# Kernel optimization log

Hardware: AMD Instinct MI355X
Metric: run time of the kernel (lower is better)

Reference implementation:

```python
import jax, jax.numpy as jnp
import numpy as np

MASK_VALUE = -10000000000.0
B, S = 2, 2048
HQ, HKV, HD = 16, 8, 256
D = HQ * HD  # 4096
ROPE_BASE = 10000.0


def rms_norm(x, scale, eps=1e-6):
    # Gemma-style RMSNorm over the last (head_dim) axis with (1 + scale) gain.
    var = jnp.mean(jnp.square(x), axis=-1, keepdims=True)
    return x * jax.lax.rsqrt(var + eps) * (1.0 + scale)


def apply_rope(x, positions):
    # x: [b, t, h, d]; positions: [b, t]
    d = x.shape[-1]
    fraction = 2.0 * jnp.arange(d // 2, dtype=jnp.float32) / d
    timescale = ROPE_BASE ** fraction                     # [d/2]
    sinusoid = positions[..., None].astype(jnp.float32) / timescale  # [b, t, d/2]
    sin = jnp.sin(sinusoid)[:, :, None, :]                # [b, t, 1, d/2]
    cos = jnp.cos(sinusoid)[:, :, None, :]
    first, second = jnp.split(x, 2, axis=-1)
    out = jnp.concatenate([first * cos - second * sin,
                           second * cos + first * sin], axis=-1)
    return out.astype(x.dtype)


def setup_inputs() -> dict:
    key = jax.random.key(0)
    ks = jax.random.split(key, 6)
    x = jax.random.normal(ks[0], (B, S, D), dtype=jnp.float32)
    Wq = jax.random.normal(ks[1], (D, HQ * HD), dtype=jnp.float32) * 0.02
    Wk = jax.random.normal(ks[2], (D, HKV * HD), dtype=jnp.float32) * 0.02
    Wv = jax.random.normal(ks[3], (D, HKV * HD), dtype=jnp.float32) * 0.02
    Wo = jax.random.normal(ks[4], (HQ * HD, D), dtype=jnp.float32) * 0.02
    k_scale = jnp.zeros((HD,), dtype=jnp.float32)
    v_scale = jnp.zeros((HD,), dtype=jnp.float32)
    mask = jnp.broadcast_to(jnp.tril(jnp.ones((S, S), dtype=bool))[None], (B, S, S))
    position = jnp.broadcast_to(jnp.arange(S, dtype=jnp.int32)[None], (B, S))
    return {"x": x, "Wq": Wq, "Wk": Wk, "Wv": Wv, "Wo": Wo,
            "k_scale": k_scale, "v_scale": v_scale,
            "mask": mask, "position": position}


def reference(x, Wq, Wk, Wv, Wo, k_scale, v_scale, mask, position):
    b, t, _ = x.shape
    group = HQ // HKV
    q = (x @ Wq).reshape(b, t, HQ, HD)
    k = (x @ Wk).reshape(b, t, HKV, HD)
    v = (x @ Wv).reshape(b, t, HKV, HD)
    k = rms_norm(k, k_scale)
    v = rms_norm(v, v_scale)
    q = apply_rope(q, position)
    k = apply_rope(k, position)
    # [b, hkv, group, t, d] view of q; avoids materializing repeated K/V (same math as repeat).
    q = q.transpose(0, 2, 1, 3).reshape(b, HKV, group, t, HD)
    k = k.transpose(0, 2, 1, 3)  # [b, hkv, T, d]
    v = v.transpose(0, 2, 1, 3)
    scores = jnp.einsum('bhgtd,bhTd->bhgtT', q, k) / jnp.sqrt(jnp.float32(HD))
    scores = jnp.where(mask[:, None, None, :, :], scores, MASK_VALUE)
    weights = jax.nn.softmax(scores, axis=-1)
    out = jnp.einsum('bhgtT,bhTd->bhgtd', weights, v)
    out = out.reshape(b, HQ, t, HD).transpose(0, 2, 1, 3).reshape(b, t, HQ * HD)
    return out @ Wo
```

## Files before the change

### kernel.cpp

```cpp
#include <hip/hip_runtime.h>
#include <stdint.h>

typedef __bf16 bf16;
typedef __bf16 bf16x4 __attribute__((ext_vector_type(4)));
typedef __bf16 bf16x8 __attribute__((ext_vector_type(8)));
typedef float f32x4 __attribute__((ext_vector_type(4)));

#define GAS __attribute__((address_space(1)))
#define LAS __attribute__((address_space(3)))

__device__ __forceinline__ void gload_lds16(const void* g, void* l) {
  __builtin_amdgcn_global_load_lds((GAS const void*)g, (LAS void*)l, 16, 0, 0);
}

__global__ __launch_bounds__(256) void cvt_bf16(const float* __restrict__ in,
                                                bf16* __restrict__ out, int n4) {
  int i = blockIdx.x * 256 + threadIdx.x;
  if (i >= n4) return;
  float4 v = ((const float4*)in)[i];
  bf16x4 o;
  o[0] = (bf16)v.x; o[1] = (bf16)v.y; o[2] = (bf16)v.z; o[3] = (bf16)v.w;
  ((bf16x4*)out)[i] = o;
}

__global__ __launch_bounds__(256) void tconv(const float* __restrict__ W,
                                             bf16* __restrict__ Wt, int K, int N) {
  __shared__ bf16 tile[64][65];
  const int tx = threadIdx.x & 63, ty = threadIdx.x >> 6;
  const int n0 = blockIdx.x * 64, k0 = blockIdx.y * 64;
#pragma unroll
  for (int i = 0; i < 16; ++i) {
    int kr = ty + i * 4;
    tile[kr][tx] = (bf16)W[(size_t)(k0 + kr) * N + n0 + tx];
  }
  __syncthreads();
#pragma unroll
  for (int i = 0; i < 16; ++i) {
    int nr = ty + i * 4;
    Wt[(size_t)(n0 + nr) * K + k0 + tx] = tile[tx][nr];
  }
}

template <int OUTF32>
__global__ __launch_bounds__(512, 2) void gemm256(const bf16* __restrict__ A,
                                                  const bf16* __restrict__ Bt,
                                                  void* __restrict__ Cp,
                                                  const int N, const int K,
                                                  const int ncc_l, const int cbx_l) {
  __shared__ __attribute__((aligned(16))) bf16 lds[2][4][8192];
  const int t = threadIdx.x, w = t >> 6, l = t & 63;
  const int la = l & 15, lq = l >> 4;
  const int xcd = blockIdx.x & 7, wi = blockIdx.x >> 3;
  const int cr = xcd >> ncc_l, cc = xcd & ((1 << ncc_l) - 1);
  const int by = (cr << 3) + (wi >> cbx_l);
  const int bx = (cc << cbx_l) + (wi & ((1 << cbx_l) - 1));
  const int m0 = by * 256, n0 = bx * 256;
  const int wr = w >> 2, wc = w & 3;
  const int c0 = w * 64 + l;
  const int sr0 = c0 >> 2, soff = (((c0 & 3) ^ ((c0 >> 3) & 3)) << 3);
  const bf16* pA0 = A + (size_t)(m0 + sr0) * K + soff;
  const bf16* pA1 = pA0 + (size_t)128 * K;
  const bf16* pB0 = Bt + (size_t)(n0 + sr0) * K + soff;
  const bf16* pB1 = pB0 + (size_t)128 * K;
  const int rsl = (lq ^ ((la >> 1) & 3)) << 3;

  f32x4 acc[8][4] = {};

#define STAGE_SLAB(s, nb, kti)                                                \
  do {                                                                        \
    const bf16* p0_ = ((s) & 1) ? pB0 : pA0;                                  \
    const bf16* p1_ = ((s) & 1) ? pB1 : pA1;                                  \
    const size_t ko_ = (size_t)(kti) * 64 + ((s) >> 1) * 32;                  \
    gload_lds16(p0_ + ko_, &lds[nb][s][w * 512]);                             \
    gload_lds16(p1_ + ko_, &lds[nb][s][4096 + w * 512]);                      \
  } while (0)

#define PHASE(kh, mg)                                                         \
  {                                                                           \
    bf16x8 a_[4];                                                             \
    _Pragma("unroll") for (int m_ = 0; m_ < 4; ++m_)                          \
        a_[m_] = *(const bf16x8*)&lds[bi][(kh)*2][(wr * 128 + (mg)*64 + m_ * 16 + la) * 32 + rsl]; \
    __builtin_amdgcn_s_setprio(1);                                            \
    _Pragma("unroll") for (int m_ = 0; m_ < 4; ++m_)                          \
      _Pragma("unroll") for (int n_ = 0; n_ < 4; ++n_)                        \
          acc[(mg)*4 + m_][n_] = __builtin_amdgcn_mfma_f32_16x16x32_bf16(     \
              a_[m_], bfr[n_], acc[(mg)*4 + m_][n_], 0, 0, 0);                \
    __builtin_amdgcn_s_setprio(0);                                            \
  }

  STAGE_SLAB(0, 0, 0);
  STAGE_SLAB(1, 0, 0);
  STAGE_SLAB(2, 0, 0);
  STAGE_SLAB(3, 0, 0);

  const int NT = K >> 6;
  for (int kt = 0; kt < NT; ++kt) {
    const int bi = kt & 1, nbi = bi ^ 1;
    const bool pf = (kt + 1) < NT;
    bf16x8 bfr[4];
    if (pf) asm volatile("s_waitcnt vmcnt(4)" ::: "memory");
    else    asm volatile("s_waitcnt vmcnt(0)" ::: "memory");
    __builtin_amdgcn_s_barrier();
    __builtin_amdgcn_sched_barrier(0);
    if (pf) STAGE_SLAB(0, nbi, kt + 1);
#pragma unroll
    for (int n_ = 0; n_ < 4; ++n_)
      bfr[n_] = *(const bf16x8*)&lds[bi][1][(wc * 64 + n_ * 16 + la) * 32 + rsl];
    PHASE(0, 0)
    if (pf) STAGE_SLAB(1, nbi, kt + 1);
    PHASE(0, 1)
    if (pf) asm volatile("s_waitcnt vmcnt(4)" ::: "memory");
    else    asm volatile("s_waitcnt vmcnt(0)" ::: "memory");
    __builtin_amdgcn_s_barrier();
    __builtin_amdgcn_sched_barrier(0);
    if (pf) STAGE_SLAB(2, nbi, kt + 1);
#pragma unroll
    for (int n_ = 0; n_ < 4; ++n_)
      bfr[n_] = *(const bf16x8*)&lds[bi][3][(wc * 64 + n_ * 16 + la) * 32 + rsl];
    PHASE(1, 0)
    if (pf) STAGE_SLAB(3, nbi, kt + 1);
    PHASE(1, 1)
  }
#undef PHASE
#undef STAGE_SLAB

  const int crow = m0 + wr * 128, ccol = n0 + wc * 64;
  if (OUTF32) {
    float* C = (float*)Cp;
#pragma unroll
    for (int mi = 0; mi < 8; ++mi)
#pragma unroll
      for (int ni = 0; ni < 4; ++ni)
#pragma unroll
        for (int i = 0; i < 4; ++i)
          C[(size_t)(crow + mi * 16 + lq * 4 + i) * N + ccol + ni * 16 + la] = acc[mi][ni][i];
  } else {
    bf16* C = (bf16*)Cp;
#pragma unroll
    for (int mi = 0; mi < 8; ++mi)
#pragma unroll
      for (int ni = 0; ni < 4; ++ni)
#pragma unroll
        for (int i = 0; i < 4; ++i)
          C[(size_t)(crow + mi * 16 + lq * 4 + i) * N + ccol + ni * 16 + la] = (bf16)acc[mi][ni][i];
  }
}

__global__ __launch_bounds__(256) void rope_q(bf16* __restrict__ qkv, const int* __restrict__ pos) {
  const int w = threadIdx.x >> 6, l = threadIdx.x & 63;
  const int idx = blockIdx.x * 4 + w;
  const int bt = idx >> 4, h = idx & 15;
  bf16* p = qkv + (size_t)bt * 8192 + h * 256 + l * 4;
  bf16x4 xv = *(const bf16x4*)p;
  float x[4], y[4];
#pragma unroll
  for (int j = 0; j < 4; ++j) x[j] = (float)xv[j];
#pragma unroll
  for (int j = 0; j < 4; ++j) y[j] = __shfl_xor(x[j], 32, 64);
  const float posf = (float)pos[bt];
  bf16x4 ov;
#pragma unroll
  for (int j = 0; j < 4; ++j) {
    const int pr = (l & 31) * 4 + j;
    float sv, cv;
    sincosf(posf * exp2f((float)pr * (-13.287712379549449f / 128.0f)), &sv, &cv);
    float o = x[j] * cv + ((l < 32) ? -y[j] : y[j]) * sv;
    ov[j] = (bf16)(o * 0.0625f);
  }
  *(bf16x4*)p = ov;
}

__global__ __launch_bounds__(256) void norm_rope_k(bf16* __restrict__ kbase,
                                                   const float* __restrict__ scale,
                                                   const int* __restrict__ pos) {
  const int w = threadIdx.x >> 6, l = threadIdx.x & 63;
  const int idx = blockIdx.x * 4 + w;
  const int bt = idx >> 3, h = idx & 7;
  bf16* p = kbase + (size_t)bt * 8192 + h * 256 + l * 4;
  bf16x4 xv = *(const bf16x4*)p;
  float x[4];
#pragma unroll
  for (int j = 0; j < 4; ++j) x[j] = (float)xv[j];
  float ss = x[0] * x[0] + x[1] * x[1] + x[2] * x[2] + x[3] * x[3];
#pragma unroll
  for (int m = 1; m < 64; m <<= 1) ss += __shfl_xor(ss, m, 64);
  const float r = rsqrtf(ss * (1.0f / 256.0f) + 1e-6f);
#pragma unroll
  for (int j = 0; j < 4; ++j) x[j] = x[j] * r * (1.0f + scale[l * 4 + j]);
  float y[4];
#pragma unroll
  for (int j = 0; j < 4; ++j) y[j] = __shfl_xor(x[j], 32, 64);
  const float posf = (float)pos[bt];
  bf16x4 ov;
#pragma unroll
  for (int j = 0; j < 4; ++j) {
    const int pr = (l & 31) * 4 + j;
    float sv, cv;
    sincosf(posf * exp2f((float)pr * (-13.287712379549449f / 128.0f)), &sv, &cv);
    float o = x[j] * cv + ((l < 32) ? -y[j] : y[j]) * sv;
    ov[j] = (bf16)o;
  }
  *(bf16x4*)p = ov;
}

__global__ __launch_bounds__(256) void norm_v(bf16* __restrict__ vbase,
                                              const float* __restrict__ scale) {
  const int w = threadIdx.x >> 6, l = threadIdx.x & 63;
  const int idx = blockIdx.x * 4 + w;
  const int bt = idx >> 3, h = idx & 7;
  bf16* p = vbase + (size_t)bt * 8192 + h * 256 + l * 4;
  bf16x4 xv = *(const bf16x4*)p;
  float x[4];
#pragma unroll
  for (int j = 0; j < 4; ++j) x[j] = (float)xv[j];
  float ss = x[0] * x[0] + x[1] * x[1] + x[2] * x[2] + x[3] * x[3];
#pragma unroll
  for (int m = 1; m < 64; m <<= 1) ss += __shfl_xor(ss, m, 64);
  const float r = rsqrtf(ss * (1.0f / 256.0f) + 1e-6f);
  bf16x4 ov;
#pragma unroll
  for (int j = 0; j < 4; ++j) ov[j] = (bf16)(x[j] * r * (1.0f + scale[l * 4 + j]));
  *(bf16x4*)p = ov;
}

__global__ __launch_bounds__(256) void vtrans(const bf16* __restrict__ vbase,
                                              bf16* __restrict__ vt) {
  __shared__ bf16 tile[64][65];
  const int tx = threadIdx.x & 63, ty = threadIdx.x >> 6;
  const int tt = blockIdx.x, dd = blockIdx.y, bh = blockIdx.z;
  const int b = bh >> 3, h = bh & 7;
#pragma unroll
  for (int i = 0; i < 16; ++i) {
    int trow = tt * 64 + ty + i * 4;
    tile[ty + i * 4][tx] = vbase[(size_t)(b * 2048 + trow) * 8192 + h * 256 + dd * 64 + tx];
  }
  __syncthreads();
#pragma unroll
  for (int i = 0; i < 16; ++i) {
    int drow = dd * 64 + ty + i * 4;
    vt[((size_t)(b * 8 + h) * 256 + drow) * 2048 + tt * 64 + tx] = tile[tx][ty + i * 4];
  }
}

__global__ __launch_bounds__(512, 2) void flash_attn(const bf16* __restrict__ qkv,
                                                     const bf16* __restrict__ vt,
                                                     bf16* __restrict__ o) {
  __shared__ __attribute__((aligned(16))) bf16 Ks[2 * 16384];
  __shared__ __attribute__((aligned(16))) bf16 Vs[2 * 16384];
  __shared__ __attribute__((aligned(16))) bf16 Ps[8 * 1152];
  const int t = threadIdx.x, w = t >> 6, l = t & 63;
  const int la = l & 15, lq = l >> 4;
  const int h = blockIdx.x, qbp = blockIdx.y, b = blockIdx.z;
  const int hkv = h >> 1;

  const bf16* kbase = qkv + (size_t)(b * 2048) * 8192 + 4096 + hkv * 256;
  const bf16* vbase = vt + ((size_t)(b * 8 + hkv)) * 256 * 2048;

  const bf16* ksrc[4];
  const bf16* vsrc[4];
#pragma unroll
  for (int i = 0; i < 4; ++i) {
    int c = i * 512 + t;
    int krr = c >> 5, ksl = (c & 31) ^ (krr & 7);
    int vrr = c >> 3, vsl = (c & 7) ^ (vrr & 7);
    ksrc[i] = kbase + (size_t)krr * 8192 + ksl * 8;
    vsrc[i] = vbase + (size_t)vrr * 2048 + vsl * 8;
  }

#define STAGE(bb, tt0)                                                        \
  do {                                                                        \
    _Pragma("unroll") for (int i_ = 0; i_ < 4; ++i_)                          \
        gload_lds16(ksrc[i_] + (size_t)(tt0) * 8192,                          \
                    Ks + (bb) * 16384 + i_ * 4096 + w * 512);                 \
    _Pragma("unroll") for (int i_ = 0; i_ < 4; ++i_)                          \
        gload_lds16(vsrc[i_] + (tt0), Vs + (bb) * 16384 + i_ * 4096 + w * 512); \
  } while (0)

  for (int part = 0; part < 2; ++part) {
    const int qb = part ? qbp : (15 - qbp);
    const int q0 = qb * 128;
    const int rbase = q0 + w * 16;

    bf16x8 qf[8];
    {
      const bf16* qrow = qkv + (size_t)(b * 2048 + rbase + la) * 8192 + h * 256 + lq * 8;
#pragma unroll
      for (int kg = 0; kg < 8; ++kg) qf[kg] = *(const bf16x8*)(qrow + kg * 32);
    }
    f32x4 acc[16] = {};
    float mrow[4] = {-1e30f, -1e30f, -1e30f, -1e30f};
    float lrow[4] = {0.f, 0.f, 0.f, 0.f};
    const int nT = 2 * qb + 2;

    STAGE(0, 0);
    int cur = 0;
    for (int tti = 0; tti < nT; ++tti) {
      const int t0 = tti * 64;
      if (tti + 1 < nT) {
        STAGE(cur ^ 1, t0 + 64);
        asm volatile("s_waitcnt vmcnt(8)" ::: "memory");
      } else {
        asm volatile("s_waitcnt vmcnt(0)" ::: "memory");
      }
      __builtin_amdgcn_s_barrier();
      __builtin_amdgcn_sched_barrier(0);
      if (t0 <= rbase + 15) {
        const bf16* Kc = Ks + cur * 16384;
        const bf16* Vc = Vs + cur * 16384;
        f32x4 s[4] = {};
        __builtin_amdgcn_s_setprio(1);
#pragma unroll
        for (int n = 0; n < 4; ++n) {
          int rT = n * 16 + la;
#pragma unroll
          for (int kg = 0; kg < 8; ++kg) {
            int sl = (kg * 4 + lq) ^ (rT & 7);
            bf16x8 kbv = *(const bf16x8*)(Kc + rT * 256 + sl * 8);
            s[n] = __builtin_amdgcn_mfma_f32_16x16x32_bf16(qf[kg], kbv, s[n], 0, 0, 0);
          }
        }
        __builtin_amdgcn_s_setprio(0);
        float scalef[4];
#pragma unroll
        for (int i = 0; i < 4; ++i) {
          const int row = rbase + lq * 4 + i;
          float mx = -1e30f;
#pragma unroll
          for (int n = 0; n < 4; ++n) {
            float v = s[n][i];
            v = (t0 + n * 16 + la > row) ? -1e30f : v;
            s[n][i] = v;
            mx = fmaxf(mx, v);
          }
          mx = fmaxf(mx, __shfl_xor(mx, 1, 64));
          mx = fmaxf(mx, __shfl_xor(mx, 2, 64));
          mx = fmaxf(mx, __shfl_xor(mx, 4, 64));
          mx = fmaxf(mx, __shfl_xor(mx, 8, 64));
          const float mnew = fmaxf(mrow[i], mx);
          scalef[i] = __expf(mrow[i] - mnew);
          float ps = 0.f;
#pragma unroll
          for (int n = 0; n < 4; ++n) {
            float v = s[n][i];
            float pp = (v <= -1e29f) ? 0.f : __expf(v - mnew);
            s[n][i] = pp;
            ps += pp;
          }
          ps += __shfl_xor(ps, 1, 64);
          ps += __shfl_xor(ps, 2, 64);
          ps += __shfl_xor(ps, 4, 64);
          ps += __shfl_xor(ps, 8, 64);
          mrow[i] = mnew;
          lrow[i] = lrow[i] * scalef[i] + ps;
        }
#pragma unroll
        for (int n = 0; n < 16; ++n) {
          acc[n][0] *= scalef[0]; acc[n][1] *= scalef[1];
          acc[n][2] *= scalef[2]; acc[n][3] *= scalef[3];
        }
        bf16* pw = Ps + w * 1152;
#pragma unroll
        for (int n = 0; n < 4; ++n)
#pragma unroll
          for (int i = 0; i < 4; ++i)
            pw[(lq * 4 + i) * 72 + n * 16 + la] = (bf16)s[n][i];
        __builtin_amdgcn_s_setprio(1);
#pragma unroll
        for (int kc = 0; kc < 2; ++kc) {
          bf16x8 pa = *(const bf16x8*)(pw + la * 72 + kc * 32 + lq * 8);
#pragma unroll
          for (int n = 0; n < 16; ++n) {
            int rd = n * 16 + la;
            int sl = (kc * 4 + lq) ^ (rd & 7);
            bf16x8 vbv = *(const bf16x8*)(Vc + rd * 64 + sl * 8);
            acc[n] = __builtin_amdgcn_mfma_f32_16x16x32_bf16(pa, vbv, acc[n], 0, 0, 0);
          }
        }
        __builtin_amdgcn_s_setprio(0);
      }
      __builtin_amdgcn_s_barrier();
      __builtin_amdgcn_sched_barrier(0);
      cur ^= 1;
    }
#pragma unroll
    for (int i = 0; i < 4; ++i) {
      const int row = rbase + lq * 4 + i;
      const float inv = 1.0f / lrow[i];
      bf16* orow = o + ((size_t)(b * 2048 + row)) * 4096 + h * 256;
#pragma unroll
      for (int n = 0; n < 16; ++n) orow[n * 16 + la] = (bf16)(acc[n][i] * inv);
    }
  }
#undef STAGE
}

__global__ void fill_err(float* o, int n) {
  int i = blockIdx.x * 256 + threadIdx.x;
  if (i < n) o[i] = 1e9f;
}

extern "C" void kernel_launch(void* const* d_in, const int* in_sizes, int n_in,
                              void* d_out, int out_size, void* d_ws, size_t ws_size,
                              hipStream_t stream) {
  const float* x = (const float*)d_in[0];
  const float* Wq = (const float*)d_in[1];
  const float* Wk = (const float*)d_in[2];
  const float* Wv = (const float*)d_in[3];
  const float* Wo = (const float*)d_in[4];
  const float* kscale = (const float*)d_in[5];
  const float* vscale = (const float*)d_in[6];
  const int* pos = (const int*)d_in[8];
  float* out = (float*)d_out;

  const size_t WS_NEED = 251658240ull;
  if (ws_size < WS_NEED) {
    fill_err<<<65536, 256, 0, stream>>>(out, out_size);
    return;
  }
  char* ws = (char*)d_ws;
  bf16* x16   = (bf16*)(ws);
  bf16* wqkvt = (bf16*)(ws + 33554432);
  bf16* wot   = (bf16*)(ws + 100663296);
  bf16* qkv   = (bf16*)(ws + 134217728);
  bf16* vtb   = (bf16*)(ws + 201326592);
  bf16* ao    = (bf16*)(ws + 218103808);

  cvt_bf16<<<16384, 256, 0, stream>>>(x, x16, 4194304);
  tconv<<<dim3(64, 64), 256, 0, stream>>>(Wq, wqkvt, 4096, 4096);
  tconv<<<dim3(32, 64), 256, 0, stream>>>(Wk, wqkvt + (size_t)4096 * 4096, 4096, 2048);
  tconv<<<dim3(32, 64), 256, 0, stream>>>(Wv, wqkvt + (size_t)6144 * 4096, 4096, 2048);
  tconv<<<dim3(64, 64), 256, 0, stream>>>(Wo, wot, 4096, 4096);

  gemm256<0><<<512, 512, 0, stream>>>(x16, wqkvt, qkv, 8192, 4096, 2, 3);

  rope_q<<<16384, 256, 0, stream>>>(qkv, pos);
  norm_rope_k<<<8192, 256, 0, stream>>>(qkv + 4096, kscale, pos);
  norm_v<<<8192, 256, 0, stream>>>(qkv + 6144, vscale);
  vtrans<<<dim3(32, 4, 16), 256, 0, stream>>>(qkv + 6144, vtb);

  flash_attn<<<dim3(16, 8, 2), 512, 0, stream>>>(qkv, vtb, ao);

  gemm256<1><<<256, 512, 0, stream>>>(ao, wot, out, 4096, 4096, 2, 2);
}
```

Before: 634.5 us.

## Share K/V tiles across GQA head pair and compute 32 query rows per wave

Restructures flash attention so each block serves one KV head and both query heads in its GQA group. Waves alternate between the two query heads, and each wave computes two 16-row query sub-tiles against every loaded K/V fragment. This halves redundant K/V staging across heads and doubles MFMA work per LDS fragment read, with 64-row query blocks, 256 threads and 1 block per CU. The cost is far more registers per wave (two accumulator sets of 16 f32x4) and less causal skipping within a tile, since the per-wave diagonal check was removed.

```diff
diff --git a/kernel.cpp b/kernel.cpp
--- a/kernel.cpp
+++ b/kernel.cpp
@@ -242,55 +242,48 @@
   }
 }
 
-__global__ __launch_bounds__(512, 2) void flash_attn(const bf16* __restrict__ qkv,
+__global__ __launch_bounds__(256, 1) void flash_attn(const bf16* __restrict__ qkv,
                                                      const bf16* __restrict__ vt,
                                                      bf16* __restrict__ o) {
   __shared__ __attribute__((aligned(16))) bf16 Ks[2 * 16384];
   __shared__ __attribute__((aligned(16))) bf16 Vs[2 * 16384];
-  __shared__ __attribute__((aligned(16))) bf16 Ps[8 * 1152];
+  __shared__ __attribute__((aligned(16))) bf16 Ps[4 * 2304];
   const int t = threadIdx.x, w = t >> 6, l = t & 63;
   const int la = l & 15, lq = l >> 4;
-  const int h = blockIdx.x, qbp = blockIdx.y, b = blockIdx.z;
-  const int hkv = h >> 1;
+  const int hkv = blockIdx.x, qp = blockIdx.y, b = blockIdx.z;
+  const int h = hkv * 2 + (w & 1);
 
   const bf16* kbase = qkv + (size_t)(b * 2048) * 8192 + 4096 + hkv * 256;
   const bf16* vbase = vt + ((size_t)(b * 8 + hkv)) * 256 * 2048;
 
-  const bf16* ksrc[4];
-  const bf16* vsrc[4];
-#pragma unroll
-  for (int i = 0; i < 4; ++i) {
-    int c = i * 512 + t;
-    int krr = c >> 5, ksl = (c & 31) ^ (krr & 7);
-    int vrr = c >> 3, vsl = (c & 7) ^ (vrr & 7);
-    ksrc[i] = kbase + (size_t)krr * 8192 + ksl * 8;
-    vsrc[i] = vbase + (size_t)vrr * 2048 + vsl * 8;
-  }
+  const bf16* ksrc = kbase + (size_t)(t >> 5) * 8192 + (((t & 31) ^ ((t >> 5) & 7)) << 3);
+  const bf16* vsrc = vbase + (size_t)(t >> 3) * 2048 + (((t & 7) ^ ((t >> 3) & 7)) << 3);
 
 #define STAGE(bb, tt0)                                                        \
   do {                                                                        \
-    _Pragma("unroll") for (int i_ = 0; i_ < 4; ++i_)                          \
-        gload_lds16(ksrc[i_] + (size_t)(tt0) * 8192,                          \
-                    Ks + (bb) * 16384 + i_ * 4096 + w * 512);                 \
-    _Pragma("unroll") for (int i_ = 0; i_ < 4; ++i_)                          \
-        gload_lds16(vsrc[i_] + (tt0), Vs + (bb) * 16384 + i_ * 4096 + w * 512); \
+    _Pragma("unroll") for (int i_ = 0; i_ < 8; ++i_)                          \
+        gload_lds16(ksrc + (size_t)((tt0) + i_ * 8) * 8192,                   \
+                    Ks + (bb) * 16384 + i_ * 2048 + t * 8);                   \
+    _Pragma("unroll") for (int i_ = 0; i_ < 8; ++i_)                          \
+        gload_lds16(vsrc + (size_t)i_ * 65536 + (tt0),                        \
+                    Vs + (bb) * 16384 + i_ * 2048 + t * 8);                   \
   } while (0)
 
   for (int part = 0; part < 2; ++part) {
-    const int qb = part ? qbp : (15 - qbp);
-    const int q0 = qb * 128;
-    const int rbase = q0 + w * 16;
-
-    bf16x8 qf[8];
-    {
-      const bf16* qrow = qkv + (size_t)(b * 2048 + rbase + la) * 8192 + h * 256 + lq * 8;
-#pragma unroll
-      for (int kg = 0; kg < 8; ++kg) qf[kg] = *(const bf16x8*)(qrow + kg * 32);
+    const int qb = part ? qp : (31 - qp);
+    const int rbase = qb * 64 + (w >> 1) * 32;
+
+    bf16x8 qf[2][8];
+#pragma unroll
+    for (int mi = 0; mi < 2; ++mi) {
+      const bf16* qrow = qkv + (size_t)(b * 2048 + rbase + mi * 16 + la) * 8192 + h * 256 + lq * 8;
+#pragma unroll
+      for (int kg = 0; kg < 8; ++kg) qf[mi][kg] = *(const bf16x8*)(qrow + kg * 32);
     }
-    f32x4 acc[16] = {};
-    float mrow[4] = {-1e30f, -1e30f, -1e30f, -1e30f};
-    float lrow[4] = {0.f, 0.f, 0.f, 0.f};
-    const int nT = 2 * qb + 2;
+    f32x4 acc[2][16] = {};
+    float mrow[2][4] = {{-1e30f, -1e30f, -1e30f, -1e30f}, {-1e30f, -1e30f, -1e30f, -1e30f}};
+    float lrow[2][4] = {};
+    const int nT = qb + 1;
 
     STAGE(0, 0);
     int cur = 0;
@@ -298,98 +291,104 @@
       const int t0 = tti * 64;
       if (tti + 1 < nT) {
         STAGE(cur ^ 1, t0 + 64);
-        asm volatile("s_waitcnt vmcnt(8)" ::: "memory");
+        asm volatile("s_waitcnt vmcnt(16)" ::: "memory");
       } else {
         asm volatile("s_waitcnt vmcnt(0)" ::: "memory");
       }
       __builtin_amdgcn_s_barrier();
       __builtin_amdgcn_sched_barrier(0);
-      if (t0 <= rbase + 15) {
-        const bf16* Kc = Ks + cur * 16384;
-        const bf16* Vc = Vs + cur * 16384;
-        f32x4 s[4] = {};
-        __builtin_amdgcn_s_setprio(1);
-#pragma unroll
-        for (int n = 0; n < 4; ++n) {
-          int rT = n * 16 + la;
-#pragma unroll
-          for (int kg = 0; kg < 8; ++kg) {
-            int sl = (kg * 4 + lq) ^ (rT & 7);
-            bf16x8 kbv = *(const bf16x8*)(Kc + rT * 256 + sl * 8);
-            s[n] = __builtin_amdgcn_mfma_f32_16x16x32_bf16(qf[kg], kbv, s[n], 0, 0, 0);
-          }
+      const bf16* Kc = Ks + cur * 16384;
+      const bf16* Vc = Vs + cur * 16384;
+      f32x4 s[2][4] = {};
+      __builtin_amdgcn_s_setprio(1);
+#pragma unroll
+      for (int n = 0; n < 4; ++n) {
+        int rT = n * 16 + la;
+#pragma unroll
+        for (int kg = 0; kg < 8; ++kg) {
+          int sl = (kg * 4 + lq) ^ (rT & 7);
+          bf16x8 kbv = *(const bf16x8*)(Kc + rT * 256 + sl * 8);
+          s[0][n] = __builtin_amdgcn_mfma_f32_16x16x32_bf16(qf[0][kg], kbv, s[0][n], 0, 0, 0);
+          s[1][n] = __builtin_amdgcn_mfma_f32_16x16x32_bf16(qf[1][kg], kbv, s[1][n], 0, 0, 0);
         }
-        __builtin_amdgcn_s_setprio(0);
+      }
+      __builtin_amdgcn_s_setprio(0);
+      bf16* pw = Ps + w * 2304;
+#pragma unroll
+      for (int mi = 0; mi < 2; ++mi) {
         float scalef[4];
 #pragma unroll
         for (int i = 0; i < 4; ++i) {
-          const int row = rbase + lq * 4 + i;
+          const int row = rbase + mi * 16 + lq * 4 + i;
           float mx = -1e30f;
 #pragma unroll
           for (int n = 0; n < 4; ++n) {
-            float v = s[n][i];
+            float v = s[mi][n][i];
             v = (t0 + n * 16 + la > row) ? -1e30f : v;
-            s[n][i] = v;
+            s[mi][n][i] = v;
             mx = fmaxf(mx, v);
           }
           mx = fmaxf(mx, __shfl_xor(mx, 1, 64));
           mx = fmaxf(mx, __shfl_xor(mx, 2, 64));
           mx = fmaxf(mx, __shfl_xor(mx, 4, 64));
           mx = fmaxf(mx, __shfl_xor(mx, 8, 64));
-          const float mnew = fmaxf(mrow[i], mx);
-          scalef[i] = __expf(mrow[i] - mnew);
+          const float mnew = fmaxf(mrow[mi][i], mx);
+          scalef[i] = __expf(mrow[mi][i] - mnew);
           float ps = 0.f;
 #pragma unroll
           for (int n = 0; n < 4; ++n) {
-            float v = s[n][i];
+            float v = s[mi][n][i];
             float pp = (v <= -1e29f) ? 0.f : __expf(v - mnew);
-            s[n][i] = pp;
+            s[mi][n][i] = pp;
             ps += pp;
           }
           ps += __shfl_xor(ps, 1, 64);
           ps += __shfl_xor(ps, 2, 64);
           ps += __shfl_xor(ps, 4, 64);
           ps += __shfl_xor(ps, 8, 64);
-          mrow[i] = mnew;
-          lrow[i] = lrow[i] * scalef[i] + ps;
+          mrow[mi][i] = mnew;
+          lrow[mi][i] = lrow[mi][i] * scalef[i] + ps;
         }
 #pragma unroll
         for (int n = 0; n < 16; ++n) {
-          acc[n][0] *= scalef[0]; acc[n][1] *= scalef[1];
-          acc[n][2] *= scalef[2]; acc[n][3] *= scalef[3];
+          acc[mi][n][0] *= scalef[0]; acc[mi][n][1] *= scalef[1];
+          acc[mi][n][2] *= scalef[2]; acc[mi][n][3] *= scalef[3];
         }
-        bf16* pw = Ps + w * 1152;
 #pragma unroll
         for (int n = 0; n < 4; ++n)
 #pragma unroll
           for (int i = 0; i < 4; ++i)
-            pw[(lq * 4 + i) * 72 + n * 16 + la] = (bf16)s[n][i];
-        __builtin_amdgcn_s_setprio(1);
-#pragma unroll
-        for (int kc = 0; kc < 2; ++kc) {
-          bf16x8 pa = *(const bf16x8*)(pw + la * 72 + kc * 32 + lq * 8);
-#pragma unroll
-          for (int n = 0; n < 16; ++n) {
-            int rd = n * 16 + la;
-            int sl = (kc * 4 + lq) ^ (rd & 7);
-            bf16x8 vbv = *(const bf16x8*)(Vc + rd * 64 + sl * 8);
-            acc[n] = __builtin_amdgcn_mfma_f32_16x16x32_bf16(pa, vbv, acc[n], 0, 0, 0);
-          }
+            pw[(mi * 16 + lq * 4 + i) * 72 + n * 16 + la] = (bf16)s[mi][n][i];
+      }
+      __builtin_amdgcn_s_setprio(1);
+#pragma unroll
+      for (int kc = 0; kc < 2; ++kc) {
+        bf16x8 pa0 = *(const bf16x8*)(pw + (la) * 72 + kc * 32 + lq * 8);
+        bf16x8 pa1 = *(const bf16x8*)(pw + (16 + la) * 72 + kc * 32 + lq * 8);
+#pragma unroll
+        for (int n = 0; n < 16; ++n) {
+          int rd = n * 16 + la;
+          int sl = (kc * 4 + lq) ^ (rd & 7);
+          bf16x8 vbv = *(const bf16x8*)(Vc + rd * 64 + sl * 8);
+          acc[0][n] = __builtin_amdgcn_mfma_f32_16x16x32_bf16(pa0, vbv, acc[0][n], 0, 0, 0);
+          acc[1][n] = __builtin_amdgcn_mfma_f32_16x16x32_bf16(pa1, vbv, acc[1][n], 0, 0, 0);
         }
-        __builtin_amdgcn_s_setprio(0);
       }
+      __builtin_amdgcn_s_setprio(0);
       __builtin_amdgcn_s_barrier();
       __builtin_amdgcn_sched_barrier(0);
       cur ^= 1;
     }
 #pragma unroll
-    for (int i = 0; i < 4; ++i) {
-      const int row = rbase + lq * 4 + i;
-      const float inv = 1.0f / lrow[i];
-      bf16* orow = o + ((size_t)(b * 2048 + row)) * 4096 + h * 256;
-#pragma unroll
-      for (int n = 0; n < 16; ++n) orow[n * 16 + la] = (bf16)(acc[n][i] * inv);
-    }
+    for (int mi = 0; mi < 2; ++mi)
+#pragma unroll
+      for (int i = 0; i < 4; ++i) {
+        const int row = rbase + mi * 16 + lq * 4 + i;
+        const float inv = 1.0f / lrow[mi][i];
+        bf16* orow = o + ((size_t)(b * 2048 + row)) * 4096 + h * 256;
+#pragma unroll
+        for (int n = 0; n < 16; ++n) orow[n * 16 + la] = (bf16)(acc[mi][n][i] * inv);
+      }
   }
 #undef STAGE
 }
@@ -438,7 +437,7 @@
   norm_v<<<8192, 256, 0, stream>>>(qkv + 6144, vscale);
   vtrans<<<dim3(32, 4, 16), 256, 0, stream>>>(qkv + 6144, vtb);
 
-  flash_attn<<<dim3(16, 8, 2), 512, 0, stream>>>(qkv, vtb, ao);
+  flash_attn<<<dim3(8, 16, 2), 256, 0, stream>>>(qkv, vtb, ao);
 
   gemm256<1><<<256, 512, 0, stream>>>(ao, wot, out, 4096, 4096, 2, 2);
 }
```

Measured after the change: 704.5 us. +11.0%, slower.

## Shrink flash-attention blocks to four waves with 32-key tiles and doubled grid

Applied to the files above, without the earlier changes.

The attention kernel now runs 256 threads (4 waves) per block, each block covering 64 query rows instead of 128, and the grid doubles along the query axis. The key/value staging tile shrinks from 64 to 32 keys, with a new swizzle for the smaller V tile. Shared memory per block roughly halves. The goal is more, smaller blocks to spread causal work more evenly across CUs and raise occupancy. The cost is twice as many loop iterations, each with barriers and less MFMA work to hide load latency.

```diff
diff --git a/kernel.cpp b/kernel.cpp
--- a/kernel.cpp
+++ b/kernel.cpp
@@ -242,44 +242,36 @@
   }
 }
 
-__global__ __launch_bounds__(512, 2) void flash_attn(const bf16* __restrict__ qkv,
+__global__ __launch_bounds__(256, 2) void flash_attn(const bf16* __restrict__ qkv,
                                                      const bf16* __restrict__ vt,
                                                      bf16* __restrict__ o) {
-  __shared__ __attribute__((aligned(16))) bf16 Ks[2 * 16384];
-  __shared__ __attribute__((aligned(16))) bf16 Vs[2 * 16384];
-  __shared__ __attribute__((aligned(16))) bf16 Ps[8 * 1152];
+  __shared__ __attribute__((aligned(16))) bf16 Ks[2 * 8192];
+  __shared__ __attribute__((aligned(16))) bf16 Vs[2 * 8192];
+  __shared__ __attribute__((aligned(16))) bf16 Ps[4 * 1152];
   const int t = threadIdx.x, w = t >> 6, l = t & 63;
   const int la = l & 15, lq = l >> 4;
-  const int h = blockIdx.x, qbp = blockIdx.y, b = blockIdx.z;
+  const int h = blockIdx.x, qp = blockIdx.y, b = blockIdx.z;
   const int hkv = h >> 1;
 
   const bf16* kbase = qkv + (size_t)(b * 2048) * 8192 + 4096 + hkv * 256;
   const bf16* vbase = vt + ((size_t)(b * 8 + hkv)) * 256 * 2048;
 
-  const bf16* ksrc[4];
-  const bf16* vsrc[4];
-#pragma unroll
-  for (int i = 0; i < 4; ++i) {
-    int c = i * 512 + t;
-    int krr = c >> 5, ksl = (c & 31) ^ (krr & 7);
-    int vrr = c >> 3, vsl = (c & 7) ^ (vrr & 7);
-    ksrc[i] = kbase + (size_t)krr * 8192 + ksl * 8;
-    vsrc[i] = vbase + (size_t)vrr * 2048 + vsl * 8;
-  }
+  const bf16* ksrc = kbase + (size_t)(t >> 5) * 8192 + (((t & 31) ^ (t >> 5)) << 3);
+  const bf16* vsrc = vbase + (size_t)(t >> 2) * 2048 + (((t & 3) ^ ((t >> 3) & 3)) << 3);
 
 #define STAGE(bb, tt0)                                                        \
   do {                                                                        \
     _Pragma("unroll") for (int i_ = 0; i_ < 4; ++i_)                          \
-        gload_lds16(ksrc[i_] + (size_t)(tt0) * 8192,                          \
-                    Ks + (bb) * 16384 + i_ * 4096 + w * 512);                 \
+        gload_lds16(ksrc + (size_t)((tt0) + i_ * 8) * 8192,                   \
+                    Ks + (bb) * 8192 + i_ * 2048 + t * 8);                    \
     _Pragma("unroll") for (int i_ = 0; i_ < 4; ++i_)                          \
-        gload_lds16(vsrc[i_] + (tt0), Vs + (bb) * 16384 + i_ * 4096 + w * 512); \
+        gload_lds16(vsrc + (size_t)(i_ * 64) * 2048 + (tt0),                  \
+                    Vs + (bb) * 8192 + i_ * 2048 + t * 8);                    \
   } while (0)
 
   for (int part = 0; part < 2; ++part) {
-    const int qb = part ? qbp : (15 - qbp);
-    const int q0 = qb * 128;
-    const int rbase = q0 + w * 16;
+    const int qb = part ? qp : (31 - qp);
+    const int rbase = qb * 64 + w * 16;
 
     bf16x8 qf[8];
     {
@@ -295,9 +287,9 @@
     STAGE(0, 0);
     int cur = 0;
     for (int tti = 0; tti < nT; ++tti) {
-      const int t0 = tti * 64;
+      const int t0 = tti * 32;
       if (tti + 1 < nT) {
-        STAGE(cur ^ 1, t0 + 64);
+        STAGE(cur ^ 1, t0 + 32);
         asm volatile("s_waitcnt vmcnt(8)" ::: "memory");
       } else {
         asm volatile("s_waitcnt vmcnt(0)" ::: "memory");
@@ -305,12 +297,12 @@
       __builtin_amdgcn_s_barrier();
       __builtin_amdgcn_sched_barrier(0);
       if (t0 <= rbase + 15) {
-        const bf16* Kc = Ks + cur * 16384;
-        const bf16* Vc = Vs + cur * 16384;
-        f32x4 s[4] = {};
+        const bf16* Kc = Ks + cur * 8192;
+        const bf16* Vc = Vs + cur * 8192;
+        f32x4 s[2] = {};
         __builtin_amdgcn_s_setprio(1);
 #pragma unroll
-        for (int n = 0; n < 4; ++n) {
+        for (int n = 0; n < 2; ++n) {
           int rT = n * 16 + la;
 #pragma unroll
           for (int kg = 0; kg < 8; ++kg) {
@@ -326,7 +318,7 @@
           const int row = rbase + lq * 4 + i;
           float mx = -1e30f;
 #pragma unroll
-          for (int n = 0; n < 4; ++n) {
+          for (int n = 0; n < 2; ++n) {
             float v = s[n][i];
             v = (t0 + n * 16 + la > row) ? -1e30f : v;
             s[n][i] = v;
@@ -340,7 +332,7 @@
           scalef[i] = __expf(mrow[i] - mnew);
           float ps = 0.f;
 #pragma unroll
-          for (int n = 0; n < 4; ++n) {
+          for (int n = 0; n < 2; ++n) {
             float v = s[n][i];
             float pp = (v <= -1e29f) ? 0.f : __expf(v - mnew);
             s[n][i] = pp;
@@ -360,19 +352,18 @@
         }
         bf16* pw = Ps + w * 1152;
 #pragma unroll
-        for (int n = 0; n < 4; ++n)
+        for (int n = 0; n < 2; ++n)
 #pragma unroll
           for (int i = 0; i < 4; ++i)
             pw[(lq * 4 + i) * 72 + n * 16 + la] = (bf16)s[n][i];
         __builtin_amdgcn_s_setprio(1);
-#pragma unroll
-        for (int kc = 0; kc < 2; ++kc) {
-          bf16x8 pa = *(const bf16x8*)(pw + la * 72 + kc * 32 + lq * 8);
+        {
+          bf16x8 pa = *(const bf16x8*)(pw + la * 72 + lq * 8);
 #pragma unroll
           for (int n = 0; n < 16; ++n) {
             int rd = n * 16 + la;
-            int sl = (kc * 4 + lq) ^ (rd & 7);
-            bf16x8 vbv = *(const bf16x8*)(Vc + rd * 64 + sl * 8);
+            int sl = lq ^ ((rd >> 1) & 3);
+            bf16x8 vbv = *(const bf16x8*)(Vc + rd * 32 + sl * 8);
             acc[n] = __builtin_amdgcn_mfma_f32_16x16x32_bf16(pa, vbv, acc[n], 0, 0, 0);
           }
         }
@@ -438,7 +429,7 @@
   norm_v<<<8192, 256, 0, stream>>>(qkv + 6144, vscale);
   vtrans<<<dim3(32, 4, 16), 256, 0, stream>>>(qkv + 6144, vtb);
 
-  flash_attn<<<dim3(16, 8, 2), 512, 0, stream>>>(qkv, vtb, ao);
+  flash_attn<<<dim3(16, 16, 2), 256, 0, stream>>>(qkv, vtb, ao);
 
   gemm256<1><<<256, 512, 0, stream>>>(ao, wot, out, 4096, 4096, 2, 2);
 }
```

New measurement: 663.2 us. 4.5% more time.

## Vectorize transpose kernels and add lazy softmax rescaling in flash attention

Applied to the files above, without the earlier changes.

The weight-conversion and V-transpose kernels now use wider vector loads and stores (float2/bf16x4) with a padded LDS tile, which cuts the number of memory transactions. In flash attention, the running max and accumulator rescale are skipped unless some row's max grows by more than a threshold anywhere in the wave (FA4-style lazy rescaling). This removes the 64 accumulator multiplies and the exps on most iterations. In exchange it adds a wave-level vote, and exp values can reach up to e^8, which risks bf16 P precision or overflow at the edges.

```diff
diff --git a/kernel.cpp b/kernel.cpp
--- a/kernel.cpp
+++ b/kernel.cpp
@@ -25,19 +25,25 @@
 
 __global__ __launch_bounds__(256) void tconv(const float* __restrict__ W,
                                              bf16* __restrict__ Wt, int K, int N) {
-  __shared__ bf16 tile[64][65];
-  const int tx = threadIdx.x & 63, ty = threadIdx.x >> 6;
+  __shared__ bf16 tile[64][68];
   const int n0 = blockIdx.x * 64, k0 = blockIdx.y * 64;
-#pragma unroll
-  for (int i = 0; i < 16; ++i) {
-    int kr = ty + i * 4;
-    tile[kr][tx] = (bf16)W[(size_t)(k0 + kr) * N + n0 + tx];
+  const int u2 = threadIdx.x & 31, kr0 = threadIdx.x >> 5;
+#pragma unroll
+  for (int i = 0; i < 8; ++i) {
+    int kr = kr0 + i * 8;
+    float2 v = *(const float2*)&W[(size_t)(k0 + kr) * N + n0 + u2 * 2];
+    tile[kr][u2 * 2] = (bf16)v.x;
+    tile[kr][u2 * 2 + 1] = (bf16)v.y;
   }
   __syncthreads();
-#pragma unroll
-  for (int i = 0; i < 16; ++i) {
-    int nr = ty + i * 4;
-    Wt[(size_t)(n0 + nr) * K + k0 + tx] = tile[tx][nr];
+  const int u4 = threadIdx.x & 15, nr0 = threadIdx.x >> 4;
+#pragma unroll
+  for (int i = 0; i < 4; ++i) {
+    int nr = nr0 + i * 16;
+    bf16x4 o;
+#pragma unroll
+    for (int j = 0; j < 4; ++j) o[j] = tile[u4 * 4 + j][nr];
+    *(bf16x4*)&Wt[(size_t)(n0 + nr) * K + k0 + u4 * 4] = o;
   }
 }
 
@@ -225,20 +231,25 @@
 
 __global__ __launch_bounds__(256) void vtrans(const bf16* __restrict__ vbase,
                                               bf16* __restrict__ vt) {
-  __shared__ bf16 tile[64][65];
-  const int tx = threadIdx.x & 63, ty = threadIdx.x >> 6;
+  __shared__ bf16 tile[64][68];
   const int tt = blockIdx.x, dd = blockIdx.y, bh = blockIdx.z;
   const int b = bh >> 3, h = bh & 7;
-#pragma unroll
-  for (int i = 0; i < 16; ++i) {
-    int trow = tt * 64 + ty + i * 4;
-    tile[ty + i * 4][tx] = vbase[(size_t)(b * 2048 + trow) * 8192 + h * 256 + dd * 64 + tx];
+  const int u4 = threadIdx.x & 15, r0 = threadIdx.x >> 4;
+#pragma unroll
+  for (int i = 0; i < 4; ++i) {
+    int tr = r0 + i * 16;
+    bf16x4 v = *(const bf16x4*)&vbase[(size_t)(b * 2048 + tt * 64 + tr) * 8192 + h * 256 + dd * 64 + u4 * 4];
+#pragma unroll
+    for (int j = 0; j < 4; ++j) tile[u4 * 4 + j][tr] = v[j];
   }
   __syncthreads();
 #pragma unroll
-  for (int i = 0; i < 16; ++i) {
-    int drow = dd * 64 + ty + i * 4;
-    vt[((size_t)(b * 8 + h) * 256 + drow) * 2048 + tt * 64 + tx] = tile[tx][ty + i * 4];
+  for (int i = 0; i < 4; ++i) {
+    int dr = r0 + i * 16;
+    bf16x4 o;
+#pragma unroll
+    for (int j = 0; j < 4; ++j) o[j] = tile[dr][u4 * 4 + j];
+    *(bf16x4*)&vt[((size_t)(b * 8 + h) * 256 + dd * 64 + dr) * 2048 + tt * 64 + u4 * 4] = o;
   }
 }
 
@@ -320,7 +331,8 @@
           }
         }
         __builtin_amdgcn_s_setprio(0);
-        float scalef[4];
+        float mxr[4];
+        float need = -1.f;
 #pragma unroll
         for (int i = 0; i < 4; ++i) {
           const int row = rbase + lq * 4 + i;
@@ -336,13 +348,26 @@
           mx = fmaxf(mx, __shfl_xor(mx, 2, 64));
           mx = fmaxf(mx, __shfl_xor(mx, 4, 64));
           mx = fmaxf(mx, __shfl_xor(mx, 8, 64));
-          const float mnew = fmaxf(mrow[i], mx);
-          scalef[i] = __expf(mrow[i] - mnew);
+          mxr[i] = mx;
+          need = fmaxf(need, mx - mrow[i]);
+        }
+        const bool resc = __any(need > 8.0f);
+        float scalef[4];
+        if (resc) {
+#pragma unroll
+          for (int i = 0; i < 4; ++i) {
+            const float mnew = fmaxf(mrow[i], mxr[i]);
+            scalef[i] = __expf(mrow[i] - mnew);
+            mrow[i] = mnew;
+          }
+        }
+#pragma unroll
+        for (int i = 0; i < 4; ++i) {
           float ps = 0.f;
 #pragma unroll
           for (int n = 0; n < 4; ++n) {
             float v = s[n][i];
-            float pp = (v <= -1e29f) ? 0.f : __expf(v - mnew);
+            float pp = (v <= -1e29f) ? 0.f : __expf(v - mrow[i]);
             s[n][i] = pp;
             ps += pp;
           }
@@ -350,13 +375,14 @@
           ps += __shfl_xor(ps, 2, 64);
           ps += __shfl_xor(ps, 4, 64);
           ps += __shfl_xor(ps, 8, 64);
-          mrow[i] = mnew;
-          lrow[i] = lrow[i] * scalef[i] + ps;
-        }
-#pragma unroll
-        for (int n = 0; n < 16; ++n) {
-          acc[n][0] *= scalef[0]; acc[n][1] *= scalef[1];
-          acc[n][2] *= scalef[2]; acc[n][3] *= scalef[3];
+          lrow[i] = resc ? (lrow[i] * scalef[i] + ps) : (lrow[i] + ps);
+        }
+        if (resc) {
+#pragma unroll
+          for (int n = 0; n < 16; ++n) {
+            acc[n][0] *= scalef[0]; acc[n][1] *= scalef[1];
+            acc[n][2] *= scalef[2]; acc[n][3] *= scalef[3];
+          }
         }
         bf16* pw = Ps + w * 1152;
 #pragma unroll
```

Measured after the change: 629.8 us, median of 2. Within noise of the previous version (-0.7%).
